# Kernel tuning notes

Hardware: AMD Instinct MI355X
Metric: run time of the kernel (lower is better)

The kernel has to match this reference:

```python
import jax, jax.numpy as jnp
import numpy as np

N_UNITS = 1024
H = 16
D_K = N_UNITS // H
B = 4
T = 2048


def setup_inputs() -> dict:
    key = jax.random.key(0)
    ks = jax.random.split(key, 9)
    scale = 1.0 / np.sqrt(N_UNITS)
    return {
        "x": jax.random.normal(ks[0], (B * T, N_UNITS), dtype=jnp.float32),
        "Wq": jax.random.normal(ks[1], (N_UNITS, N_UNITS), dtype=jnp.float32) * scale,
        "bq": jax.random.normal(ks[2], (N_UNITS,), dtype=jnp.float32) * 0.01,
        "Wk": jax.random.normal(ks[3], (N_UNITS, N_UNITS), dtype=jnp.float32) * scale,
        "bk": jax.random.normal(ks[4], (N_UNITS,), dtype=jnp.float32) * 0.01,
        "Wv": jax.random.normal(ks[5], (N_UNITS, N_UNITS), dtype=jnp.float32) * scale,
        "bv": jax.random.normal(ks[6], (N_UNITS,), dtype=jnp.float32) * 0.01,
        "Wo": jax.random.normal(ks[7], (N_UNITS, N_UNITS), dtype=jnp.float32) * scale,
        "bo": jax.random.normal(ks[8], (N_UNITS,), dtype=jnp.float32) * 0.01,
        "batch_size": B,
    }


def reference(x, Wq, bq, Wk, bk, Wv, bv, Wo, bo, batch_size):
    # x: (batch*seq, n_units). Project then split into heads.
    q = (x @ Wq.T + bq).reshape(batch_size, -1, H, D_K)  # (b, t, h, d)
    k = (x @ Wk.T + bk).reshape(batch_size, -1, H, D_K)
    v = (x @ Wv.T + bv).reshape(batch_size, -1, H, D_K)
    scores = jnp.einsum("bqhd,bkhd->bhqk", q, k) / np.sqrt(D_K)
    att = jax.nn.softmax(scores, axis=-1)  # dropout=0.0 -> identity
    ctx = jnp.einsum("bhqk,bkhd->bqhd", att, v)
    ctx = ctx.reshape(-1, H * D_K)  # (batch*seq, n_units)
    return ctx @ Wo.T + bo
```

## Files before the change

### kernel.cpp

```cpp
#include <hip/hip_runtime.h>

typedef __bf16 bf16_t;
typedef __attribute__((ext_vector_type(8))) __bf16 bf16x8;
typedef __attribute__((ext_vector_type(4))) __bf16 bf16x4;
typedef __attribute__((ext_vector_type(4))) float f32x4;

#define M_TOT 8192
#define NU    1024
#define TSEQ  2048
#define NHEAD 16
#define DHEAD 64
#define BPAD  72
#define QSCALE 0.18033688011f

__device__ __forceinline__ void gload_lds16(const void* g, void* lds) {
    __builtin_amdgcn_global_load_lds(
        (const __attribute__((address_space(1))) void*)g,
        (__attribute__((address_space(3))) void*)lds,
        16, 0, 0);
}

__device__ __forceinline__ unsigned pk2(float a, float b) {
    const bf16_t x = (bf16_t)a, y = (bf16_t)b;
    return (unsigned)__builtin_bit_cast(unsigned short, x)
         | ((unsigned)__builtin_bit_cast(unsigned short, y) << 16);
}

__device__ __forceinline__ int fidx(int r, int k) {
    return ((((r >> 4) & 3) * 2 + (k >> 5)) << 9)
         + (((((k >> 3) & 3) << 4) + (r & 15)) << 3) + (k & 7);
}
__device__ __forceinline__ size_t fragK(int bh, int t, int d) {
    return (size_t)bh * (TSEQ * DHEAD) + (size_t)(t >> 6) * 4096 + fidx(t & 63, d);
}
__device__ __forceinline__ size_t fragV(int bh, int t, int d) {
    return (size_t)bh * (TSEQ * DHEAD) + (size_t)(t >> 6) * 4096 + fidx(d, t & 63);
}

__global__ __launch_bounds__(256)
void cvt_x(const float* __restrict__ x, bf16_t* __restrict__ xb)
{
    const int i = (blockIdx.x * 256 + threadIdx.x) * 8;
    const float4 a = *(const float4*)(x + i);
    const float4 b = *(const float4*)(x + i + 4);
    bf16x8 v;
    v[0] = (bf16_t)a.x; v[1] = (bf16_t)a.y; v[2] = (bf16_t)a.z; v[3] = (bf16_t)a.w;
    v[4] = (bf16_t)b.x; v[5] = (bf16_t)b.y; v[6] = (bf16_t)b.z; v[7] = (bf16_t)b.w;
    *(bf16x8*)(xb + i) = v;
}

__global__ __launch_bounds__(256)
void cvt_frag(const float* __restrict__ src, bf16_t* __restrict__ dst)
{
    const int o8   = blockIdx.x * 256 + threadIdx.x;
    const int tile = o8 >> 9;
    const int c    = (o8 >> 6) & 7;
    const int s    = o8 & 63;
    const int r  = (tile >> 4) * 64 + ((c >> 1) * 16 + (s & 15));
    const int k  = (tile & 15) * 64 + ((c & 1) * 32 + ((s >> 4) * 8));
    const float4 a = *(const float4*)(src + (size_t)r * NU + k);
    const float4 b = *(const float4*)(src + (size_t)r * NU + k + 4);
    bf16x8 v;
    v[0] = (bf16_t)a.x; v[1] = (bf16_t)a.y; v[2] = (bf16_t)a.z; v[3] = (bf16_t)a.w;
    v[4] = (bf16_t)b.x; v[5] = (bf16_t)b.y; v[6] = (bf16_t)b.z; v[7] = (bf16_t)b.w;
    *(bf16x8*)(dst + (size_t)o8 * 8) = v;
}

__global__ __launch_bounds__(256)
void gemm_qkv_f(const bf16_t* __restrict__ xf,
                const bf16_t* __restrict__ Wqf, const bf16_t* __restrict__ Wkf, const bf16_t* __restrict__ Wvf,
                const float* __restrict__ B0, const float* __restrict__ B1, const float* __restrict__ B2,
                bf16_t* __restrict__ O0, bf16_t* __restrict__ O1, bf16_t* __restrict__ O2)
{
    const int z = blockIdx.z;
    const bf16_t* Wf  = (z == 0) ? Wqf : (z == 1 ? Wkf : Wvf);
    const float* bias = (z == 0) ? B0 : (z == 1 ? B1 : B2);
    bf16_t* out       = (z == 0) ? O0 : (z == 1 ? O1 : O2);
    const float scale = (z == 0) ? QSCALE : 1.0f;

    __shared__ __attribute__((aligned(16))) bf16_t As[2 * 4096];
    __shared__ __attribute__((aligned(16))) bf16_t Bs[2 * 4096];

    const int tid = threadIdx.x;
    const int l   = tid & 63;
    const int w   = tid >> 6;
    const int wm  = w >> 1, wn = w & 1;
    const int l15 = l & 15, lq = l >> 4;
    const int bm  = blockIdx.y, bn = blockIdx.x;

    const bf16_t* gA[4];
    const bf16_t* gB[4];
#pragma unroll
    for (int i = 0; i < 4; ++i) {
        const int cc = w * 4 + i;
        gA[i] = xf + ((size_t)(bm * 2 + (cc >> 3)) * 16) * 4096 + (cc & 7) * 512 + l * 8;
        gB[i] = Wf + ((size_t)(bn * 2 + (cc >> 3)) * 16) * 4096 + (cc & 7) * 512 + l * 8;
    }

    f32x4 acc[4][4] = {};

    for (int kt = 0; kt < 16; ++kt) {
#pragma unroll
        for (int i = 0; i < 4; ++i) {
            const int cc = w * 4 + i;
            gload_lds16(gA[i] + (size_t)kt * 4096, &As[cc * 512]);
            gload_lds16(gB[i] + (size_t)kt * 4096, &Bs[cc * 512]);
        }
        __syncthreads();
#pragma unroll
        for (int ks = 0; ks < 2; ++ks) {
            bf16x8 af[4], bfr[4];
#pragma unroll
            for (int mt = 0; mt < 4; ++mt)
                af[mt] = *(const bf16x8*)&As[wm * 4096 + (mt * 2 + ks) * 512 + l * 8];
#pragma unroll
            for (int nt = 0; nt < 4; ++nt)
                bfr[nt] = *(const bf16x8*)&Bs[wn * 4096 + (nt * 2 + ks) * 512 + l * 8];
#pragma unroll
            for (int mt = 0; mt < 4; ++mt)
#pragma unroll
                for (int nt = 0; nt < 4; ++nt)
                    acc[mt][nt] = __builtin_amdgcn_mfma_f32_16x16x32_bf16(af[mt], bfr[nt], acc[mt][nt], 0, 0, 0);
        }
        __syncthreads();
    }

#pragma unroll
    for (int nt = 0; nt < 4; ++nt) {
        const int gn = bn * 128 + wn * 64 + nt * 16 + l15;
        const float bv = bias[gn];
#pragma unroll
        for (int mt = 0; mt < 4; ++mt) {
            const int rb = bm * 128 + wm * 64 + mt * 16 + lq * 4;
#pragma unroll
            for (int r = 0; r < 4; ++r) {
                const int gm = rb + r;
                const float v = (acc[mt][nt][r] + bv) * scale;
                const int b = gm >> 11, t = gm & (TSEQ - 1);
                const int h = gn >> 6,  d = gn & 63;
                const int bh = b * NHEAD + h;
                if (z == 0)
                    out[((size_t)bh * TSEQ + t) * DHEAD + d] = (bf16_t)v;
                else if (z == 1)
                    out[fragK(bh, t, d)] = (bf16_t)v;
                else
                    out[fragV(bh, t, d)] = (bf16_t)v;
            }
        }
    }
}

__global__ __launch_bounds__(256)
void gemm_out_f(const bf16_t* __restrict__ cf, const bf16_t* __restrict__ Wof,
                const float* __restrict__ bo, float* __restrict__ out)
{
    __shared__ __attribute__((aligned(16))) bf16_t As[2 * 4096];
    __shared__ __attribute__((aligned(16))) bf16_t Bs[2 * 4096];

    const int tid = threadIdx.x;
    const int l   = tid & 63;
    const int w   = tid >> 6;
    const int wm  = w >> 1, wn = w & 1;
    const int l15 = l & 15, lq = l >> 4;
    const int bm  = blockIdx.y, bn = blockIdx.x;
    const int b   = bm >> 4;

    const bf16_t* gB[4];
    size_t aoff[4];
#pragma unroll
    for (int i = 0; i < 4; ++i) {
        const int cc = w * 4 + i;
        aoff[i] = (((size_t)b * 16) * 32 + (bm & 15) * 2 + (cc >> 3)) * 4096 + (cc & 7) * 512 + l * 8;
        gB[i] = Wof + ((size_t)(bn * 2 + (cc >> 3)) * 16) * 4096 + (cc & 7) * 512 + l * 8;
    }

    f32x4 acc[4][4] = {};

    for (int kt = 0; kt < 16; ++kt) {
#pragma unroll
        for (int i = 0; i < 4; ++i) {
            const int cc = w * 4 + i;
            gload_lds16(cf + aoff[i] + (size_t)kt * (32 * 4096), &As[cc * 512]);
            gload_lds16(gB[i] + (size_t)kt * 4096, &Bs[cc * 512]);
        }
        __syncthreads();
#pragma unroll
        for (int ks = 0; ks < 2; ++ks) {
            bf16x8 af[4], bfr[4];
#pragma unroll
            for (int mt = 0; mt < 4; ++mt)
                af[mt] = *(const bf16x8*)&As[wm * 4096 + (mt * 2 + ks) * 512 + l * 8];
#pragma unroll
            for (int nt = 0; nt < 4; ++nt)
                bfr[nt] = *(const bf16x8*)&Bs[wn * 4096 + (nt * 2 + ks) * 512 + l * 8];
#pragma unroll
            for (int mt = 0; mt < 4; ++mt)
#pragma unroll
                for (int nt = 0; nt < 4; ++nt)
                    acc[mt][nt] = __builtin_amdgcn_mfma_f32_16x16x32_bf16(af[mt], bfr[nt], acc[mt][nt], 0, 0, 0);
        }
        __syncthreads();
    }

#pragma unroll
    for (int nt = 0; nt < 4; ++nt) {
        const int gn = bn * 128 + wn * 64 + nt * 16 + l15;
        const float bv = bo[gn];
#pragma unroll
        for (int mt = 0; mt < 4; ++mt) {
            const int rb = bm * 128 + wm * 64 + mt * 16 + lq * 4;
#pragma unroll
            for (int r = 0; r < 4; ++r)
                out[(size_t)(rb + r) * NU + gn] = acc[mt][nt][r] + bv;
        }
    }
}

__global__ __launch_bounds__(256)
void gemm_qkv(const bf16_t* __restrict__ A,
              const float* __restrict__ W0, const float* __restrict__ W1, const float* __restrict__ W2,
              const float* __restrict__ B0, const float* __restrict__ B1, const float* __restrict__ B2,
              bf16_t* __restrict__ O0, bf16_t* __restrict__ O1, bf16_t* __restrict__ O2)
{
    const int z = blockIdx.z;
    const float* W    = (z == 0) ? W0 : (z == 1 ? W1 : W2);
    const float* bias = (z == 0) ? B0 : (z == 1 ? B1 : B2);
    bf16_t* out       = (z == 0) ? O0 : (z == 1 ? O1 : O2);
    const float scale = (z == 0) ? QSCALE : 1.0f;

    __shared__ __attribute__((aligned(16))) bf16_t As[128 * 64];
    __shared__ __attribute__((aligned(16))) bf16_t Bs[128 * BPAD];

    const int tid = threadIdx.x;
    const int l = tid & 63, w = tid >> 6;
    const int wm = w >> 1, wn = w & 1;
    const int l15 = l & 15, lq = l >> 4;
    const int bm = blockIdx.y, bn = blockIdx.x;
    const int srow = l >> 3, scol = (l & 7) * 8;
    const bf16_t* gA = A + (size_t)(bm * 128 + srow) * NU + scol;
    const int sr = tid >> 4, sc = (tid & 15) * 4;
    const float* gW = W + (size_t)(bn * 128 + sr) * NU + sc;

    f32x4 acc[4][4] = {};
    float4 wreg[8];
#pragma unroll
    for (int i = 0; i < 8; ++i) wreg[i] = *(const float4*)(gW + (size_t)(i * 16) * NU);

    for (int k0 = 0; k0 < NU; k0 += 64) {
#pragma unroll
        for (int i = 0; i < 4; ++i) {
            const int r0 = i * 32 + w * 8;
            gload_lds16(gA + (size_t)r0 * NU + k0, &As[r0 * 64]);
        }
#pragma unroll
        for (int i = 0; i < 8; ++i) {
            bf16x4 wb;
            wb[0] = (bf16_t)wreg[i].x; wb[1] = (bf16_t)wreg[i].y;
            wb[2] = (bf16_t)wreg[i].z; wb[3] = (bf16_t)wreg[i].w;
            *(bf16x4*)&Bs[(i * 16 + sr) * BPAD + sc] = wb;
        }
        __syncthreads();
        if (k0 + 64 < NU) {
#pragma unroll
            for (int i = 0; i < 8; ++i)
                wreg[i] = *(const float4*)(gW + (size_t)(i * 16) * NU + k0 + 64);
        }
#pragma unroll
        for (int ks = 0; ks < 2; ++ks) {
            bf16x8 af[4], bfr[4];
#pragma unroll
            for (int mt = 0; mt < 4; ++mt)
                af[mt] = *(const bf16x8*)&As[(wm * 64 + mt * 16 + l15) * 64 + ks * 32 + lq * 8];
#pragma unroll
            for (int nt = 0; nt < 4; ++nt)
                bfr[nt] = *(const bf16x8*)&Bs[(wn * 64 + nt * 16 + l15) * BPAD + ks * 32 + lq * 8];
#pragma unroll
            for (int mt = 0; mt < 4; ++mt)
#pragma unroll
                for (int nt = 0; nt < 4; ++nt)
                    acc[mt][nt] = __builtin_amdgcn_mfma_f32_16x16x32_bf16(af[mt], bfr[nt], acc[mt][nt], 0, 0, 0);
        }
        __syncthreads();
    }

#pragma unroll
    for (int nt = 0; nt < 4; ++nt) {
        const int gn = bn * 128 + wn * 64 + nt * 16 + l15;
        const float bv = bias[gn];
#pragma unroll
        for (int mt = 0; mt < 4; ++mt) {
            const int rb = bm * 128 + wm * 64 + mt * 16 + lq * 4;
#pragma unroll
            for (int r = 0; r < 4; ++r) {
                const int gm = rb + r;
                const float v = (acc[mt][nt][r] + bv) * scale;
                const int b = gm >> 11, t = gm & (TSEQ - 1);
                const int h = gn >> 6,  d = gn & 63;
                const int bh = b * NHEAD + h;
                if (z == 0)      out[((size_t)bh * TSEQ + t) * DHEAD + d] = (bf16_t)v;
                else if (z == 1) out[fragK(bh, t, d)] = (bf16_t)v;
                else             out[fragV(bh, t, d)] = (bf16_t)v;
            }
        }
    }
}

__global__ __launch_bounds__(256)
void gemm_out(const bf16_t* __restrict__ ctx, const float* __restrict__ Wo,
              const float* __restrict__ bo, float* __restrict__ out)
{
    __shared__ __attribute__((aligned(16))) bf16_t As[128 * 64];
    __shared__ __attribute__((aligned(16))) bf16_t Bs[128 * BPAD];

    const int tid = threadIdx.x;
    const int l = tid & 63, w = tid >> 6;
    const int wm = w >> 1, wn = w & 1;
    const int l15 = l & 15, lq = l >> 4;
    const int bm = blockIdx.y, bn = blockIdx.x;
    const int srow = l >> 3, scol = (l & 7) * 8;
    const int b = bm >> 4;
    const bf16_t* gA = ctx + (size_t)b * (NHEAD * TSEQ * DHEAD)
                           + (size_t)((bm & 15) * 128 + srow) * DHEAD + scol;
    const int sr = tid >> 4, sc = (tid & 15) * 4;
    const float* gW = Wo + (size_t)(bn * 128 + sr) * NU + sc;

    f32x4 acc[4][4] = {};
    float4 wreg[8];
#pragma unroll
    for (int i = 0; i < 8; ++i) wreg[i] = *(const float4*)(gW + (size_t)(i * 16) * NU);

    for (int k0 = 0; k0 < NU; k0 += 64) {
#pragma unroll
        for (int i = 0; i < 4; ++i) {
            const int r0 = i * 32 + w * 8;
            gload_lds16(gA + (size_t)r0 * DHEAD + ((size_t)k0 << 11), &As[r0 * 64]);
        }
#pragma unroll
        for (int i = 0; i < 8; ++i) {
            bf16x4 wb;
            wb[0] = (bf16_t)wreg[i].x; wb[1] = (bf16_t)wreg[i].y;
            wb[2] = (bf16_t)wreg[i].z; wb[3] = (bf16_t)wreg[i].w;
            *(bf16x4*)&Bs[(i * 16 + sr) * BPAD + sc] = wb;
        }
        __syncthreads();
        if (k0 + 64 < NU) {
#pragma unroll
            for (int i = 0; i < 8; ++i)
                wreg[i] = *(const float4*)(gW + (size_t)(i * 16) * NU + k0 + 64);
        }
#pragma unroll
        for (int ks = 0; ks < 2; ++ks) {
            bf16x8 af[4], bfr[4];
#pragma unroll
            for (int mt = 0; mt < 4; ++mt)
                af[mt] = *(const bf16x8*)&As[(wm * 64 + mt * 16 + l15) * 64 + ks * 32 + lq * 8];
#pragma unroll
            for (int nt = 0; nt < 4; ++nt)
                bfr[nt] = *(const bf16x8*)&Bs[(wn * 64 + nt * 16 + l15) * BPAD + ks * 32 + lq * 8];
#pragma unroll
            for (int mt = 0; mt < 4; ++mt)
#pragma unroll
                for (int nt = 0; nt < 4; ++nt)
                    acc[mt][nt] = __builtin_amdgcn_mfma_f32_16x16x32_bf16(af[mt], bfr[nt], acc[mt][nt], 0, 0, 0);
        }
        __syncthreads();
    }

#pragma unroll
    for (int nt = 0; nt < 4; ++nt) {
        const int gn = bn * 128 + wn * 64 + nt * 16 + l15;
        const float bv = bo[gn];
#pragma unroll
        for (int mt = 0; mt < 4; ++mt) {
            const int rb = bm * 128 + wm * 64 + mt * 16 + lq * 4;
#pragma unroll
            for (int r = 0; r < 4; ++r)
                out[(size_t)(rb + r) * NU + gn] = acc[mt][nt][r] + bv;
        }
    }
}

template <bool FRAGOUT>
__global__ __launch_bounds__(256)
void attn_fwd(const bf16_t* __restrict__ Q, const bf16_t* __restrict__ Kf,
              const bf16_t* __restrict__ Vf, bf16_t* __restrict__ Cw)
{
    __shared__ __attribute__((aligned(16))) bf16_t Ks[8 * 512];
    __shared__ __attribute__((aligned(16))) bf16_t Vs[8 * 512];
    __shared__ __attribute__((aligned(16))) bf16_t Ps[4][4 * 512];

    const int tid = threadIdx.x;
    const int l   = tid & 63;
    const int w   = tid >> 6;
    const int l15 = l & 15, lq = l >> 4;
    const int bh  = blockIdx.y;
    const int q0  = blockIdx.x * 128 + w * 32;

    const bf16_t* Qb = Q  + (size_t)bh * TSEQ * DHEAD;
    const bf16_t* Kb = Kf + (size_t)bh * TSEQ * DHEAD;
    const bf16_t* Vb = Vf + (size_t)bh * TSEQ * DHEAD;

    bf16x8 qf[2][2];
#pragma unroll
    for (int mt = 0; mt < 2; ++mt)
#pragma unroll
        for (int ks = 0; ks < 2; ++ks)
            qf[mt][ks] = *(const bf16x8*)(Qb + (size_t)(q0 + mt * 16 + l15) * DHEAD + ks * 32 + lq * 8);

    bf16x8 ones;
#pragma unroll
    for (int j = 0; j < 8; ++j) ones[j] = (bf16_t)1.0f;

    f32x4 cacc[2][4] = {};
    f32x4 lacc[2] = {};

    int* PsI = (int*)&Ps[w][0];

    for (int kt = 0; kt < TSEQ / 64; ++kt) {
        const bf16_t* kb = Kb + kt * 4096;
        const bf16_t* vb = Vb + kt * 4096;
        gload_lds16(kb + (w * 2 + 0) * 512 + l * 8, &Ks[(w * 2 + 0) * 512]);
        gload_lds16(kb + (w * 2 + 1) * 512 + l * 8, &Ks[(w * 2 + 1) * 512]);
        gload_lds16(vb + (w * 2 + 0) * 512 + l * 8, &Vs[(w * 2 + 0) * 512]);
        gload_lds16(vb + (w * 2 + 1) * 512 + l * 8, &Vs[(w * 2 + 1) * 512]);
        __syncthreads();

        f32x4 st[4][2] = {};
#pragma unroll
        for (int ks = 0; ks < 2; ++ks) {
            bf16x8 kf[4];
#pragma unroll
            for (int nt = 0; nt < 4; ++nt)
                kf[nt] = *(const bf16x8*)&Ks[(nt * 2 + ks) * 512 + l * 8];
#pragma unroll
            for (int nt = 0; nt < 4; ++nt)
#pragma unroll
                for (int mt = 0; mt < 2; ++mt)
                    st[nt][mt] = __builtin_amdgcn_mfma_f32_16x16x32_bf16(kf[nt], qf[mt][ks], st[nt][mt], 0, 0, 0);
        }

#pragma unroll
        for (int nt = 0; nt < 4; ++nt)
#pragma unroll
            for (int mt = 0; mt < 2; ++mt) {
                const float p0 = __builtin_amdgcn_exp2f(st[nt][mt][0]);
                const float p1 = __builtin_amdgcn_exp2f(st[nt][mt][1]);
                const float p2 = __builtin_amdgcn_exp2f(st[nt][mt][2]);
                const float p3 = __builtin_amdgcn_exp2f(st[nt][mt][3]);
                const int base = (mt * 2 + (nt >> 1)) * 256
                               + ((nt & 1) * 2 + (lq >> 1)) * 64 + l15 * 4;
                PsI[base + ((lq * 2 + 0) & 3)] = (int)pk2(p0, p1);
                PsI[base + ((lq * 2 + 1) & 3)] = (int)pk2(p2, p3);
            }

#pragma unroll
        for (int kv = 0; kv < 2; ++kv) {
            bf16x8 vf[4], pf[2];
#pragma unroll
            for (int dt = 0; dt < 4; ++dt)
                vf[dt] = *(const bf16x8*)&Vs[(dt * 2 + kv) * 512 + l * 8];
#pragma unroll
            for (int mt = 0; mt < 2; ++mt)
                pf[mt] = *(const bf16x8*)&Ps[w][(mt * 2 + kv) * 512 + l * 8];
#pragma unroll
            for (int mt = 0; mt < 2; ++mt) {
                lacc[mt] = __builtin_amdgcn_mfma_f32_16x16x32_bf16(ones, pf[mt], lacc[mt], 0, 0, 0);
#pragma unroll
                for (int dt = 0; dt < 4; ++dt)
                    cacc[mt][dt] = __builtin_amdgcn_mfma_f32_16x16x32_bf16(vf[dt], pf[mt], cacc[mt][dt], 0, 0, 0);
            }
        }
        __syncthreads();
    }

#pragma unroll
    for (int mt = 0; mt < 2; ++mt) {
        const float inv = 1.0f / lacc[mt][0];
        const int q = q0 + mt * 16 + l15;
#pragma unroll
        for (int dt = 0; dt < 4; ++dt) {
            bf16x4 cv;
#pragma unroll
            for (int r = 0; r < 4; ++r) cv[r] = (bf16_t)(cacc[mt][dt][r] * inv);
            if (FRAGOUT) {
                const int qr = q & 63;
                const size_t base = ((size_t)bh * 32 + (q >> 6)) * 4096;
                const int d0 = dt * 16 + lq * 4;
                const int addr = ((((qr >> 4) & 3) * 2 + (d0 >> 5)) << 9)
                               + (((((d0 >> 3) & 3) << 4) + (qr & 15)) << 3) + (d0 & 7);
                *(bf16x4*)&Cw[base + addr] = cv;
            } else {
                *(bf16x4*)&Cw[((size_t)bh * TSEQ + q) * DHEAD + dt * 16 + lq * 4] = cv;
            }
        }
    }
}

__global__ void diag_fill(float* out, int n, float val)
{
    int i = blockIdx.x * blockDim.x + threadIdx.x;
    if (i < n) out[i] = val;
}

extern "C" void kernel_launch(void* const* d_in, const int* in_sizes, int n_in,
                              void* d_out, int out_size, void* d_ws, size_t ws_size,
                              hipStream_t stream)
{
    const float* x  = (const float*)d_in[0];
    const float* Wq = (const float*)d_in[1];
    const float* bq = (const float*)d_in[2];
    const float* Wk = (const float*)d_in[3];
    const float* bk = (const float*)d_in[4];
    const float* Wv = (const float*)d_in[5];
    const float* bv = (const float*)d_in[6];
    const float* Wo = (const float*)d_in[7];
    const float* bo = (const float*)d_in[8];

    const size_t SLOT = (size_t)M_TOT * NU;
    const size_t WSZ  = (size_t)NU * NU;
    const size_t need_fast = (2 * SLOT + 4 * WSZ) * sizeof(bf16_t);
    const size_t need_min  = 2 * SLOT * sizeof(bf16_t);

    bf16_t* Qw = (bf16_t*)d_out;
    bf16_t* Kw = Qw + SLOT;

    if (ws_size >= need_fast) {
        bf16_t* Xf  = (bf16_t*)d_ws;
        bf16_t* Vt  = Xf + SLOT;
        bf16_t* Wqf = Vt + SLOT;
        bf16_t* Wkf = Wqf + WSZ;
        bf16_t* Wvf = Wkf + WSZ;
        bf16_t* Wof = Wvf + WSZ;
        bf16_t* Cf  = Xf;

        cvt_frag<<<dim3(M_TOT * NU / (256 * 8)), 256, 0, stream>>>(x,  Xf);
        cvt_frag<<<dim3(NU * NU / (256 * 8)),    256, 0, stream>>>(Wq, Wqf);
        cvt_frag<<<dim3(NU * NU / (256 * 8)),    256, 0, stream>>>(Wk, Wkf);
        cvt_frag<<<dim3(NU * NU / (256 * 8)),    256, 0, stream>>>(Wv, Wvf);
        cvt_frag<<<dim3(NU * NU / (256 * 8)),    256, 0, stream>>>(Wo, Wof);
        gemm_qkv_f<<<dim3(NU / 128, M_TOT / 128, 3), 256, 0, stream>>>(
            Xf, Wqf, Wkf, Wvf, bq, bk, bv, Qw, Kw, Vt);
        attn_fwd<true><<<dim3(TSEQ / 128, 64), 256, 0, stream>>>(Qw, Kw, Vt, Cf);
        gemm_out_f<<<dim3(NU / 128, M_TOT / 128), 256, 0, stream>>>(Cf, Wof, bo, (float*)d_out);
    } else if (ws_size >= need_min) {
        bf16_t* Xb = (bf16_t*)d_ws;
        bf16_t* Vt = Xb + SLOT;
        bf16_t* Cw = Xb;
        cvt_x<<<dim3(M_TOT * NU / (256 * 8)), 256, 0, stream>>>(x, Xb);
        gemm_qkv<<<dim3(NU / 128, M_TOT / 128, 3), 256, 0, stream>>>(
            Xb, Wq, Wk, Wv, bq, bk, bv, Qw, Kw, Vt);
        attn_fwd<false><<<dim3(TSEQ / 128, 64), 256, 0, stream>>>(Qw, Kw, Vt, Cw);
        gemm_out<<<dim3(NU / 128, M_TOT / 128), 256, 0, stream>>>(Cw, Wo, bo, (float*)d_out);
    } else {
        diag_fill<<<(out_size + 255) / 256, 256, 0, stream>>>((float*)d_out, out_size, 9.0f);
    }
}
```

Baseline: 314.4 us.

## Load K/V fragments directly into registers and remap attention block order

The attention kernel no longer stages K and V tiles in shared memory. Each wave now loads its pre-fragmented K/V tiles straight from global memory into registers, which removes two block barriers per key tile. The grid is flattened to 1024 blocks with a swizzled mapping that spreads the (batch, head) pairs across XCDs, and launch bounds now request 3 blocks per CU. The four weight-conversion launches are also merged into one z-indexed launch. The trade-off is that every wave now fetches K/V redundantly, so global/L2 traffic rises fourfold, and register pressure grows.

```diff
diff --git a/kernel.cpp b/kernel.cpp
--- a/kernel.cpp
+++ b/kernel.cpp
@@ -49,8 +49,7 @@
     *(bf16x8*)(xb + i) = v;
 }
 
-__global__ __launch_bounds__(256)
-void cvt_frag(const float* __restrict__ src, bf16_t* __restrict__ dst)
+__device__ __forceinline__ void cvt_frag_body(const float* __restrict__ src, bf16_t* __restrict__ dst)
 {
     const int o8   = blockIdx.x * 256 + threadIdx.x;
     const int tile = o8 >> 9;
@@ -64,6 +63,22 @@
     v[0] = (bf16_t)a.x; v[1] = (bf16_t)a.y; v[2] = (bf16_t)a.z; v[3] = (bf16_t)a.w;
     v[4] = (bf16_t)b.x; v[5] = (bf16_t)b.y; v[6] = (bf16_t)b.z; v[7] = (bf16_t)b.w;
     *(bf16x8*)(dst + (size_t)o8 * 8) = v;
+}
+
+__global__ __launch_bounds__(256)
+void cvt_frag(const float* __restrict__ src, bf16_t* __restrict__ dst)
+{
+    cvt_frag_body(src, dst);
+}
+
+__global__ __launch_bounds__(256)
+void cvt_frag_w(const float* __restrict__ Wq, const float* __restrict__ Wk,
+                const float* __restrict__ Wv, const float* __restrict__ Wo,
+                bf16_t* __restrict__ dst)
+{
+    const int z = blockIdx.z;
+    const float* src = (z == 0) ? Wq : (z == 1 ? Wk : (z == 2 ? Wv : Wo));
+    cvt_frag_body(src, dst + (size_t)z * NU * NU);
 }
 
 __global__ __launch_bounds__(256)
@@ -381,24 +396,25 @@
 }
 
 template <bool FRAGOUT>
-__global__ __launch_bounds__(256)
+__global__ __launch_bounds__(256, 3)
 void attn_fwd(const bf16_t* __restrict__ Q, const bf16_t* __restrict__ Kf,
               const bf16_t* __restrict__ Vf, bf16_t* __restrict__ Cw)
 {
-    __shared__ __attribute__((aligned(16))) bf16_t Ks[8 * 512];
-    __shared__ __attribute__((aligned(16))) bf16_t Vs[8 * 512];
     __shared__ __attribute__((aligned(16))) bf16_t Ps[4][4 * 512];
 
     const int tid = threadIdx.x;
     const int l   = tid & 63;
     const int w   = tid >> 6;
     const int l15 = l & 15, lq = l >> 4;
-    const int bh  = blockIdx.y;
-    const int q0  = blockIdx.x * 128 + w * 32;
+
+    const int id = blockIdx.x;
+    const int bh = (id & 7) * 8 + ((id >> 3) & 7);
+    const int qt = id >> 6;
+    const int q0 = qt * 128 + w * 32;
 
     const bf16_t* Qb = Q  + (size_t)bh * TSEQ * DHEAD;
-    const bf16_t* Kb = Kf + (size_t)bh * TSEQ * DHEAD;
-    const bf16_t* Vb = Vf + (size_t)bh * TSEQ * DHEAD;
+    const bf16_t* Kb = Kf + (size_t)bh * TSEQ * DHEAD + l * 8;
+    const bf16_t* Vb = Vf + (size_t)bh * TSEQ * DHEAD + l * 8;
 
     bf16x8 qf[2][2];
 #pragma unroll
@@ -419,25 +435,19 @@
     for (int kt = 0; kt < TSEQ / 64; ++kt) {
         const bf16_t* kb = Kb + kt * 4096;
         const bf16_t* vb = Vb + kt * 4096;
-        gload_lds16(kb + (w * 2 + 0) * 512 + l * 8, &Ks[(w * 2 + 0) * 512]);
-        gload_lds16(kb + (w * 2 + 1) * 512 + l * 8, &Ks[(w * 2 + 1) * 512]);
-        gload_lds16(vb + (w * 2 + 0) * 512 + l * 8, &Vs[(w * 2 + 0) * 512]);
-        gload_lds16(vb + (w * 2 + 1) * 512 + l * 8, &Vs[(w * 2 + 1) * 512]);
-        __syncthreads();
+
+        bf16x8 kf[8];
+#pragma unroll
+        for (int c = 0; c < 8; ++c) kf[c] = *(const bf16x8*)(kb + c * 512);
 
         f32x4 st[4][2] = {};
 #pragma unroll
-        for (int ks = 0; ks < 2; ++ks) {
-            bf16x8 kf[4];
+        for (int ks = 0; ks < 2; ++ks)
 #pragma unroll
             for (int nt = 0; nt < 4; ++nt)
-                kf[nt] = *(const bf16x8*)&Ks[(nt * 2 + ks) * 512 + l * 8];
-#pragma unroll
-            for (int nt = 0; nt < 4; ++nt)
 #pragma unroll
                 for (int mt = 0; mt < 2; ++mt)
-                    st[nt][mt] = __builtin_amdgcn_mfma_f32_16x16x32_bf16(kf[nt], qf[mt][ks], st[nt][mt], 0, 0, 0);
-        }
+                    st[nt][mt] = __builtin_amdgcn_mfma_f32_16x16x32_bf16(kf[nt * 2 + ks], qf[mt][ks], st[nt][mt], 0, 0, 0);
 
 #pragma unroll
         for (int nt = 0; nt < 4; ++nt)
@@ -453,12 +463,13 @@
                 PsI[base + ((lq * 2 + 1) & 3)] = (int)pk2(p2, p3);
             }
 
+        bf16x8 vf[8];
+#pragma unroll
+        for (int c = 0; c < 8; ++c) vf[c] = *(const bf16x8*)(vb + c * 512);
+
 #pragma unroll
         for (int kv = 0; kv < 2; ++kv) {
-            bf16x8 vf[4], pf[2];
-#pragma unroll
-            for (int dt = 0; dt < 4; ++dt)
-                vf[dt] = *(const bf16x8*)&Vs[(dt * 2 + kv) * 512 + l * 8];
+            bf16x8 pf[2];
 #pragma unroll
             for (int mt = 0; mt < 2; ++mt)
                 pf[mt] = *(const bf16x8*)&Ps[w][(mt * 2 + kv) * 512 + l * 8];
@@ -467,10 +478,9 @@
                 lacc[mt] = __builtin_amdgcn_mfma_f32_16x16x32_bf16(ones, pf[mt], lacc[mt], 0, 0, 0);
 #pragma unroll
                 for (int dt = 0; dt < 4; ++dt)
-                    cacc[mt][dt] = __builtin_amdgcn_mfma_f32_16x16x32_bf16(vf[dt], pf[mt], cacc[mt][dt], 0, 0, 0);
+                    cacc[mt][dt] = __builtin_amdgcn_mfma_f32_16x16x32_bf16(vf[dt * 2 + kv], pf[mt], cacc[mt][dt], 0, 0, 0);
             }
         }
-        __syncthreads();
     }
 
 #pragma unroll
@@ -527,21 +537,15 @@
     if (ws_size >= need_fast) {
         bf16_t* Xf  = (bf16_t*)d_ws;
         bf16_t* Vt  = Xf + SLOT;
-        bf16_t* Wqf = Vt + SLOT;
-        bf16_t* Wkf = Wqf + WSZ;
-        bf16_t* Wvf = Wkf + WSZ;
-        bf16_t* Wof = Wvf + WSZ;
+        bf16_t* Wf4 = Vt + SLOT;
         bf16_t* Cf  = Xf;
 
-        cvt_frag<<<dim3(M_TOT * NU / (256 * 8)), 256, 0, stream>>>(x,  Xf);
-        cvt_frag<<<dim3(NU * NU / (256 * 8)),    256, 0, stream>>>(Wq, Wqf);
-        cvt_frag<<<dim3(NU * NU / (256 * 8)),    256, 0, stream>>>(Wk, Wkf);
-        cvt_frag<<<dim3(NU * NU / (256 * 8)),    256, 0, stream>>>(Wv, Wvf);
-        cvt_frag<<<dim3(NU * NU / (256 * 8)),    256, 0, stream>>>(Wo, Wof);
+        cvt_frag<<<dim3(M_TOT * NU / (256 * 8)), 256, 0, stream>>>(x, Xf);
+        cvt_frag_w<<<dim3(NU * NU / (256 * 8), 1, 4), 256, 0, stream>>>(Wq, Wk, Wv, Wo, Wf4);
         gemm_qkv_f<<<dim3(NU / 128, M_TOT / 128, 3), 256, 0, stream>>>(
-            Xf, Wqf, Wkf, Wvf, bq, bk, bv, Qw, Kw, Vt);
-        attn_fwd<true><<<dim3(TSEQ / 128, 64), 256, 0, stream>>>(Qw, Kw, Vt, Cf);
-        gemm_out_f<<<dim3(NU / 128, M_TOT / 128), 256, 0, stream>>>(Cf, Wof, bo, (float*)d_out);
+            Xf, Wf4, Wf4 + WSZ, Wf4 + 2 * WSZ, bq, bk, bv, Qw, Kw, Vt);
+        attn_fwd<true><<<dim3(1024), 256, 0, stream>>>(Qw, Kw, Vt, Cf);
+        gemm_out_f<<<dim3(NU / 128, M_TOT / 128), 256, 0, stream>>>(Cf, Wf4 + 3 * WSZ, bo, (float*)d_out);
     } else if (ws_size >= need_min) {
         bf16_t* Xb = (bf16_t*)d_ws;
         bf16_t* Vt = Xb + SLOT;
@@ -549,7 +553,7 @@
         cvt_x<<<dim3(M_TOT * NU / (256 * 8)), 256, 0, stream>>>(x, Xb);
         gemm_qkv<<<dim3(NU / 128, M_TOT / 128, 3), 256, 0, stream>>>(
             Xb, Wq, Wk, Wv, bq, bk, bv, Qw, Kw, Vt);
-        attn_fwd<false><<<dim3(TSEQ / 128, 64), 256, 0, stream>>>(Qw, Kw, Vt, Cw);
+        attn_fwd<false><<<dim3(1024), 256, 0, stream>>>(Qw, Kw, Vt, Cw);
         gemm_out<<<dim3(NU / 128, M_TOT / 128), 256, 0, stream>>>(Cw, Wo, bo, (float*)d_out);
     } else {
         diag_fill<<<(out_size + 255) / 256, 256, 0, stream>>>((float*)d_out, out_size, 9.0f);
```

After: 286.2 us. 9.0% less time.
